# Kernel tuning notes

Hardware: AMD Instinct MI355X
Metric: run time of the kernel (lower is better)

## Reference

```python
import jax, jax.numpy as jnp
import numpy as np

IN_FEATURES = 4096
OUT_FEATURES = 11008
W_BITS = 4
GROUP_SIZE = 128
NUM_CHERRIES = 128                       # ceil(4096*0.03125)//8*8
NUM_NORMAL = IN_FEATURES - NUM_CHERRIES  # 3968
N_GROUPS = NUM_NORMAL // GROUP_SIZE      # 31
QROWS = NUM_NORMAL // 8 * W_BITS         # 1984 packed uint8 rows
QMIN = -(2 ** (W_BITS - 1))              # signed int4 min = -8
BATCH = 64


def setup_inputs() -> dict:
    key = jax.random.key(0)
    k1, k2, k3, k4, k5 = jax.random.split(key, 5)
    x = jax.random.normal(k1, (BATCH, IN_FEATURES), jnp.float32)
    # packed 4-bit weights: two nibbles per uint8, stored as [QROWS, out]
    qweight = jax.random.randint(k2, (QROWS, OUT_FEATURES), 0, 256, jnp.int32).astype(jnp.uint8)
    # per-group scales, stored transposed as [n_groups, out]
    scales = jax.random.uniform(k3, (N_GROUPS, OUT_FEATURES), jnp.float32, 0.005, 0.02)
    # full-precision outlier ('cherry') columns, stored as [num_cherries, out]
    cherry_weight = jax.random.normal(k4, (NUM_CHERRIES, OUT_FEATURES), jnp.float32) * 0.02
    rng = np.random.default_rng(0)
    cherry_indices = jnp.asarray(
        np.sort(rng.choice(IN_FEATURES, NUM_CHERRIES, replace=False)).astype(np.int32))
    bias = jax.random.normal(k5, (OUT_FEATURES,), jnp.float32) * 0.01
    return {"x": x, "qweight": qweight, "cherry_weight": cherry_weight,
            "cherry_indices": cherry_indices, "scales": scales, "bias": bias}


def _normal_indices(cherry_indices):
    # complement of cherry_indices, as in the torch scatter/nonzero construction
    mask = jnp.ones((IN_FEATURES,), dtype=bool).at[cherry_indices].set(False)
    return jnp.nonzero(mask, size=NUM_NORMAL)[0]  # static size -> jit ok


def reference(x, qweight, cherry_weight, cherry_indices, scales, bias):
    # --- unpack 4-bit weights (matches QuantLinear.unpack for w_bits=4) ---
    q = qweight.T                                    # [out, QROWS]
    nib = jnp.stack([q & 0xF, (q >> 4) & 0xF], axis=-1)  # low nibble first
    nib = nib.reshape(OUT_FEATURES, NUM_NORMAL)
    intw = nib.astype(jnp.int32) + QMIN              # signed int4 values
    # --- dequantize: repeat-interleave per-group scales along in dim ---
    s = jnp.repeat(scales.T, GROUP_SIZE, axis=1)     # [out, NUM_NORMAL]
    w_normal = intw.astype(s.dtype) * s              # dequantized normal weight
    # --- merge cherry outlier columns via column-gather on x (same math as
    #     scattering into a full [out, in] weight then x @ W.T) ---
    normal_idx = _normal_indices(cherry_indices)
    out = x[:, normal_idx] @ w_normal.T + x[:, cherry_indices] @ cherry_weight
    return out + bias
```

## Files before the change

### kernel.cpp

```cpp
#include <hip/hip_runtime.h>
#include <hip/hip_bf16.h>
#include <stdint.h>

#define IN_F 4096
#define OUT_F 11008
#define NUM_CH 128
#define NUM_NORM 3968
#define BATCH 64
#define KSPLIT 8
#define KCHUNK (IN_F / KSPLIT)
#define NMEGA (KCHUNK / 128)
#define BS 136

typedef short short8 __attribute__((ext_vector_type(8)));
typedef float float4v __attribute__((ext_vector_type(4)));
typedef int int4v __attribute__((ext_vector_type(4)));

__device__ __forceinline__ unsigned short f2bf(float f) {
    union { float f; unsigned u; } v; v.f = f;
    unsigned u = v.u;
    return (unsigned short)((u + 0x7FFFu + ((u >> 16) & 1u)) >> 16);
}

__device__ __forceinline__ unsigned pk_bf16(float lo, float hi) {
    __hip_bfloat162 h = __float22bfloat162_rn(make_float2(lo, hi));
    union { __hip_bfloat162 h; unsigned u; } c; c.h = h; return c.u;
}

__global__ __launch_bounds__(256) void init_out(
        const float* __restrict__ bias, float* __restrict__ out) {
    const int i = blockIdx.x * 256 + threadIdx.x;
    const int c = i % (OUT_F / 4);
    const float4v b4 = *reinterpret_cast<const float4v*>(bias + c * 4);
    reinterpret_cast<float4v*>(out)[i] = b4;
}

__global__ __launch_bounds__(256) void permute_x(
        const float* __restrict__ x, const int* __restrict__ cidx,
        unsigned short* __restrict__ xp) {
    int i = blockIdx.x * blockDim.x + threadIdx.x;
    int b = blockIdx.y;
    int lo = 0, hi = NUM_CH;
    while (lo < hi) { int mid = (lo + hi) >> 1; if (cidx[mid] < i) lo = mid + 1; else hi = mid; }
    bool isch = (lo < NUM_CH) && (cidx[lo] == i);
    int pos = isch ? (NUM_NORM + lo) : (i - lo);
    xp[b * IN_F + pos] = f2bf(x[b * IN_F + i]);
}

__global__ __launch_bounds__(256, 3) void qgemm(
        const unsigned short* __restrict__ xp, const int* __restrict__ qw,
        const float* __restrict__ cw, const float* __restrict__ scales,
        float* __restrict__ out) {
    __shared__ unsigned short Bt[4][32][BS];

    const int tid  = threadIdx.x;
    const int wave = tid >> 6;
    const int lane = tid & 63;
    const int ln   = lane & 15;
    const int lq   = lane >> 4;
    const int c4   = (lane & 7) * 4;
    const int rg   = lane >> 3;

    const int n0w   = (blockIdx.x * 4 + wave) * 32;
    const int kbase = blockIdx.y * KCHUNK;

    unsigned short (*tile)[BS] = Bt[wave];

    const int*   qcolp = qw + n0w + c4;
    const float* scolp = scales + n0w + c4;
    const float* ccolp = cw + n0w + c4;

    float4v acc[4][2];
    #pragma unroll
    for (int mt = 0; mt < 4; ++mt)
        #pragma unroll
        for (int nf = 0; nf < 2; ++nf) acc[mt][nf] = (float4v){0.f, 0.f, 0.f, 0.f};

    int4v qcur[8]; float4v scur;
    {
        const size_t rb = (size_t)(kbase >> 1) + rg * 8;
        #pragma unroll
        for (int i = 0; i < 8; ++i)
            qcur[i] = *reinterpret_cast<const int4v*>(qcolp + (rb + i) * OUT_F);
        scur = *reinterpret_cast<const float4v*>(scolp + (size_t)(kbase >> 7) * OUT_F);
    }

    for (int s = 0; s < NMEGA; ++s) {
        const int k0 = kbase + s * 128;

        if (k0 < NUM_NORM) {
            int4v q[8]; const float4v sc = scur;
            #pragma unroll
            for (int i = 0; i < 8; ++i) q[i] = qcur[i];
            const int kn = k0 + 128;
            if (s + 1 < NMEGA && kn < NUM_NORM) {
                const size_t rb = (size_t)(kn >> 1) + rg * 8;
                #pragma unroll
                for (int i = 0; i < 8; ++i)
                    qcur[i] = *reinterpret_cast<const int4v*>(qcolp + (rb + i) * OUT_F);
                scur = *reinterpret_cast<const float4v*>(scolp + (size_t)(kn >> 7) * OUT_F);
            }
            #pragma unroll
            for (int j = 0; j < 4; ++j) {
                const float s1 = sc[j];
                #pragma unroll
                for (int p = 0; p < 2; ++p) {
                    union { short8 v; unsigned u[4]; } wv;
                    #pragma unroll
                    for (int m = 0; m < 4; ++m) {
                        const int qq = q[p * 4 + m][j];
                        wv.u[m] = pk_bf16((float)((qq & 0xF) - 8) * s1,
                                          (float)(((qq >> 4) & 0xF) - 8) * s1);
                    }
                    *reinterpret_cast<short8*>(&tile[c4 + j][rg * 16 + p * 8]) = wv.v;
                }
            }
        } else {
            float4v chv[16];
            #pragma unroll
            for (int t = 0; t < 16; ++t)
                chv[t] = *reinterpret_cast<const float4v*>(
                    ccolp + (size_t)(rg * 16 + t) * OUT_F);
            #pragma unroll
            for (int j = 0; j < 4; ++j) {
                #pragma unroll
                for (int p = 0; p < 2; ++p) {
                    union { short8 v; unsigned u[4]; } wv;
                    #pragma unroll
                    for (int m = 0; m < 4; ++m)
                        wv.u[m] = pk_bf16(chv[p * 8 + 2 * m][j], chv[p * 8 + 2 * m + 1][j]);
                    *reinterpret_cast<short8*>(&tile[c4 + j][rg * 16 + p * 8]) = wv.v;
                }
            }
        }

        short8 a_sub[4];
        #pragma unroll
        for (int mt = 0; mt < 4; ++mt)
            a_sub[mt] = *reinterpret_cast<const short8*>(
                xp + (size_t)(mt * 16 + ln) * IN_F + k0 + (lq << 3));

        #pragma unroll
        for (int sub = 0; sub < 4; ++sub) {
            const short8 b0 = *reinterpret_cast<const short8*>(
                &tile[ln][sub * 32 + (lq << 3)]);
            const short8 b1 = *reinterpret_cast<const short8*>(
                &tile[16 + ln][sub * 32 + (lq << 3)]);
            short8 a_nxt[4];
            if (sub < 3) {
                #pragma unroll
                for (int mt = 0; mt < 4; ++mt)
                    a_nxt[mt] = *reinterpret_cast<const short8*>(
                        xp + (size_t)(mt * 16 + ln) * IN_F + k0 + (sub + 1) * 32 + (lq << 3));
            }
            #pragma unroll
            for (int mt = 0; mt < 4; ++mt) {
                acc[mt][0] = __builtin_amdgcn_mfma_f32_16x16x32_bf16(a_sub[mt], b0, acc[mt][0], 0, 0, 0);
                acc[mt][1] = __builtin_amdgcn_mfma_f32_16x16x32_bf16(a_sub[mt], b1, acc[mt][1], 0, 0, 0);
            }
            if (sub < 3) {
                #pragma unroll
                for (int mt = 0; mt < 4; ++mt) a_sub[mt] = a_nxt[mt];
            }
        }
    }

    #pragma unroll
    for (int mt = 0; mt < 4; ++mt) {
        #pragma unroll
        for (int nf = 0; nf < 2; ++nf) {
            const int n = n0w + nf * 16 + ln;
            #pragma unroll
            for (int r = 0; r < 4; ++r) {
                const int m = mt * 16 + (lq << 2) + r;
                atomicAdd(&out[(size_t)m * OUT_F + n], acc[mt][nf][r]);
            }
        }
    }
}

extern "C" void kernel_launch(void* const* d_in, const int* in_sizes, int n_in,
                              void* d_out, int out_size, void* d_ws, size_t ws_size,
                              hipStream_t stream) {
    const float* x      = (const float*)d_in[0];
    const int*   qw     = (const int*)d_in[1];
    const float* cw     = (const float*)d_in[2];
    const int*   cidx   = (const int*)d_in[3];
    const float* scales = (const float*)d_in[4];
    const float* bias   = (const float*)d_in[5];
    float*       out    = (float*)d_out;
    unsigned short* xp  = (unsigned short*)d_ws;

    init_out<<<(BATCH * OUT_F / 4) / 256, 256, 0, stream>>>(bias, out);
    dim3 pgrid(IN_F / 256, BATCH);
    permute_x<<<pgrid, 256, 0, stream>>>(x, cidx, xp);
    qgemm<<<dim3(OUT_F / 128, KSPLIT), 256, 0, stream>>>(xp, qw, cw, scales, out);
}
```

Baseline: 174.8 us.

## Repack weights into MFMA-friendly layout and dequantize directly in registers

Adds two pre-pass kernels that run on every call. One packs the 4-bit weights so that each output column's 16 K-bytes sit contiguously; the other converts the cherry weights to bf16 in a matching per-column layout. The GEMM then loads each lane's B fragment straight from global memory into registers, dequantizes it there and feeds the MFMAs, with no LDS tile and no strided column loads. The cost is an extra full pass over the original weights plus writing and re-reading the packed copy, traded for better-coalesced streaming and a simpler inner loop.

```diff
diff --git a/kernel.cpp b/kernel.cpp
--- a/kernel.cpp
+++ b/kernel.cpp
@@ -7,14 +7,14 @@
 #define NUM_CH 128
 #define NUM_NORM 3968
 #define BATCH 64
+#define KB_N 124
 #define KSPLIT 8
-#define KCHUNK (IN_F / KSPLIT)
-#define NMEGA (KCHUNK / 128)
-#define BS 136
+#define KCHUNK 512
+#define NSUB 16
 
 typedef short short8 __attribute__((ext_vector_type(8)));
 typedef float float4v __attribute__((ext_vector_type(4)));
-typedef int int4v __attribute__((ext_vector_type(4)));
+typedef unsigned uint4v __attribute__((ext_vector_type(4)));
 
 __device__ __forceinline__ unsigned short f2bf(float f) {
     union { float f; unsigned u; } v; v.f = f;
@@ -47,28 +47,84 @@
     xp[b * IN_F + pos] = f2bf(x[b * IN_F + i]);
 }
 
-__global__ __launch_bounds__(256, 3) void qgemm(
-        const unsigned short* __restrict__ xp, const int* __restrict__ qw,
-        const float* __restrict__ cw, const float* __restrict__ scales,
+__global__ __launch_bounds__(256) void repack_n(
+        const int* __restrict__ qw, unsigned char* __restrict__ pk) {
+    const int kb = blockIdx.y;
+    const int n  = blockIdx.x * 256 + threadIdx.x;
+    const int* src = qw + (size_t)kb * 16 * OUT_F + n;
+    unsigned dw[4];
+    #pragma unroll
+    for (int a = 0; a < 4; ++a) {
+        const unsigned b0 = (unsigned)src[(size_t)(4 * a + 0) * OUT_F] & 0xFFu;
+        const unsigned b1 = (unsigned)src[(size_t)(4 * a + 1) * OUT_F] & 0xFFu;
+        const unsigned b2 = (unsigned)src[(size_t)(4 * a + 2) * OUT_F] & 0xFFu;
+        const unsigned b3 = (unsigned)src[(size_t)(4 * a + 3) * OUT_F] & 0xFFu;
+        dw[a] = b0 | (b1 << 8) | (b2 << 16) | (b3 << 24);
+    }
+    *reinterpret_cast<uint4v*>(pk + ((size_t)kb * OUT_F + n) * 16) =
+        (uint4v){dw[0], dw[1], dw[2], dw[3]};
+}
+
+__global__ __launch_bounds__(256) void repack_ch(
+        const float* __restrict__ cw, unsigned short* __restrict__ pkc) {
+    const int kbc = blockIdx.y;
+    const int n   = blockIdx.x * 256 + threadIdx.x;
+    const float* src = cw + (size_t)kbc * 32 * OUT_F + n;
+    unsigned u[16];
+    #pragma unroll
+    for (int j = 0; j < 16; ++j)
+        u[j] = pk_bf16(src[(size_t)(2 * j) * OUT_F], src[(size_t)(2 * j + 1) * OUT_F]);
+    uint4v* dst = reinterpret_cast<uint4v*>(pkc + ((size_t)kbc * OUT_F + n) * 32);
+    #pragma unroll
+    for (int q = 0; q < 4; ++q)
+        dst[q] = (uint4v){u[4 * q], u[4 * q + 1], u[4 * q + 2], u[4 * q + 3]};
+}
+
+__global__ __launch_bounds__(256) void qgemm(
+        const unsigned short* __restrict__ xp, const unsigned* __restrict__ pk,
+        const unsigned short* __restrict__ pkc, const float* __restrict__ scales,
         float* __restrict__ out) {
-    __shared__ unsigned short Bt[4][32][BS];
-
     const int tid  = threadIdx.x;
     const int wave = tid >> 6;
     const int lane = tid & 63;
     const int ln   = lane & 15;
     const int lq   = lane >> 4;
-    const int c4   = (lane & 7) * 4;
-    const int rg   = lane >> 3;
-
-    const int n0w   = (blockIdx.x * 4 + wave) * 32;
-    const int kbase = blockIdx.y * KCHUNK;
-
-    unsigned short (*tile)[BS] = Bt[wave];
-
-    const int*   qcolp = qw + n0w + c4;
-    const float* scolp = scales + n0w + c4;
-    const float* ccolp = cw + n0w + c4;
+    const int n0w  = (blockIdx.x * 4 + wave) * 32;
+    const int ky   = blockIdx.y;
+    const int kbase = ky * KCHUNK;
+    const int kb0   = ky * 16;
+    const bool chblk = (ky == KSPLIT - 1);
+    const int nsubn  = chblk ? 12 : 16;
+
+    const int nc0 = n0w + ln;
+    const int nc1 = n0w + 16 + ln;
+
+    unsigned bq[16][2];
+    #pragma unroll
+    for (int sub = 0; sub < 16; ++sub) {
+        if (sub < nsubn) {
+            bq[sub][0] = pk[((size_t)(kb0 + sub) * OUT_F + nc0) * 4 + lq];
+            bq[sub][1] = pk[((size_t)(kb0 + sub) * OUT_F + nc1) * 4 + lq];
+        }
+    }
+    short8 cb[4][2];
+    if (chblk) {
+        #pragma unroll
+        for (int s4 = 0; s4 < 4; ++s4) {
+            cb[s4][0] = *reinterpret_cast<const short8*>(
+                pkc + ((size_t)s4 * OUT_F + nc0) * 32 + lq * 8);
+            cb[s4][1] = *reinterpret_cast<const short8*>(
+                pkc + ((size_t)s4 * OUT_F + nc1) * 32 + lq * 8);
+        }
+    }
+    float sc[4][2];
+    #pragma unroll
+    for (int gi = 0; gi < 4; ++gi) {
+        if (gi * 4 < nsubn) {
+            sc[gi][0] = scales[(size_t)(ky * 4 + gi) * OUT_F + nc0];
+            sc[gi][1] = scales[(size_t)(ky * 4 + gi) * OUT_F + nc1];
+        }
+    }
 
     float4v acc[4][2];
     #pragma unroll
@@ -76,92 +132,45 @@
         #pragma unroll
         for (int nf = 0; nf < 2; ++nf) acc[mt][nf] = (float4v){0.f, 0.f, 0.f, 0.f};
 
-    int4v qcur[8]; float4v scur;
-    {
-        const size_t rb = (size_t)(kbase >> 1) + rg * 8;
-        #pragma unroll
-        for (int i = 0; i < 8; ++i)
-            qcur[i] = *reinterpret_cast<const int4v*>(qcolp + (rb + i) * OUT_F);
-        scur = *reinterpret_cast<const float4v*>(scolp + (size_t)(kbase >> 7) * OUT_F);
-    }
-
-    for (int s = 0; s < NMEGA; ++s) {
-        const int k0 = kbase + s * 128;
-
-        if (k0 < NUM_NORM) {
-            int4v q[8]; const float4v sc = scur;
-            #pragma unroll
-            for (int i = 0; i < 8; ++i) q[i] = qcur[i];
-            const int kn = k0 + 128;
-            if (s + 1 < NMEGA && kn < NUM_NORM) {
-                const size_t rb = (size_t)(kn >> 1) + rg * 8;
-                #pragma unroll
-                for (int i = 0; i < 8; ++i)
-                    qcur[i] = *reinterpret_cast<const int4v*>(qcolp + (rb + i) * OUT_F);
-                scur = *reinterpret_cast<const float4v*>(scolp + (size_t)(kn >> 7) * OUT_F);
+    const unsigned short* xpb = xp + kbase + lq * 8;
+    short8 a_cur[4], a_nxt[4];
+    #pragma unroll
+    for (int mt = 0; mt < 4; ++mt)
+        a_cur[mt] = *reinterpret_cast<const short8*>(xpb + (size_t)(mt * 16 + ln) * IN_F);
+
+    #pragma unroll
+    for (int sub = 0; sub < 16; ++sub) {
+        short8 bf0, bf1;
+        if (!chblk || sub < 12) {
+            const float s0 = sc[sub >> 2][0], s1 = sc[sub >> 2][1];
+            union { short8 v; unsigned u[4]; } w0, w1;
+            #pragma unroll
+            for (int i = 0; i < 4; ++i) {
+                const unsigned y0 = (bq[sub][0] >> (8 * i)) & 0xFFu;
+                const unsigned y1 = (bq[sub][1] >> (8 * i)) & 0xFFu;
+                w0.u[i] = pk_bf16((float)((int)(y0 & 0xFu) - 8) * s0,
+                                  (float)((int)(y0 >> 4) - 8) * s0);
+                w1.u[i] = pk_bf16((float)((int)(y1 & 0xFu) - 8) * s1,
+                                  (float)((int)(y1 >> 4) - 8) * s1);
             }
-            #pragma unroll
-            for (int j = 0; j < 4; ++j) {
-                const float s1 = sc[j];
-                #pragma unroll
-                for (int p = 0; p < 2; ++p) {
-                    union { short8 v; unsigned u[4]; } wv;
-                    #pragma unroll
-                    for (int m = 0; m < 4; ++m) {
-                        const int qq = q[p * 4 + m][j];
-                        wv.u[m] = pk_bf16((float)((qq & 0xF) - 8) * s1,
-                                          (float)(((qq >> 4) & 0xF) - 8) * s1);
-                    }
-                    *reinterpret_cast<short8*>(&tile[c4 + j][rg * 16 + p * 8]) = wv.v;
-                }
-            }
+            bf0 = w0.v; bf1 = w1.v;
         } else {
-            float4v chv[16];
-            #pragma unroll
-            for (int t = 0; t < 16; ++t)
-                chv[t] = *reinterpret_cast<const float4v*>(
-                    ccolp + (size_t)(rg * 16 + t) * OUT_F);
-            #pragma unroll
-            for (int j = 0; j < 4; ++j) {
-                #pragma unroll
-                for (int p = 0; p < 2; ++p) {
-                    union { short8 v; unsigned u[4]; } wv;
-                    #pragma unroll
-                    for (int m = 0; m < 4; ++m)
-                        wv.u[m] = pk_bf16(chv[p * 8 + 2 * m][j], chv[p * 8 + 2 * m + 1][j]);
-                    *reinterpret_cast<short8*>(&tile[c4 + j][rg * 16 + p * 8]) = wv.v;
-                }
-            }
-        }
-
-        short8 a_sub[4];
-        #pragma unroll
-        for (int mt = 0; mt < 4; ++mt)
-            a_sub[mt] = *reinterpret_cast<const short8*>(
-                xp + (size_t)(mt * 16 + ln) * IN_F + k0 + (lq << 3));
-
-        #pragma unroll
-        for (int sub = 0; sub < 4; ++sub) {
-            const short8 b0 = *reinterpret_cast<const short8*>(
-                &tile[ln][sub * 32 + (lq << 3)]);
-            const short8 b1 = *reinterpret_cast<const short8*>(
-                &tile[16 + ln][sub * 32 + (lq << 3)]);
-            short8 a_nxt[4];
-            if (sub < 3) {
-                #pragma unroll
-                for (int mt = 0; mt < 4; ++mt)
-                    a_nxt[mt] = *reinterpret_cast<const short8*>(
-                        xp + (size_t)(mt * 16 + ln) * IN_F + k0 + (sub + 1) * 32 + (lq << 3));
-            }
-            #pragma unroll
-            for (int mt = 0; mt < 4; ++mt) {
-                acc[mt][0] = __builtin_amdgcn_mfma_f32_16x16x32_bf16(a_sub[mt], b0, acc[mt][0], 0, 0, 0);
-                acc[mt][1] = __builtin_amdgcn_mfma_f32_16x16x32_bf16(a_sub[mt], b1, acc[mt][1], 0, 0, 0);
-            }
-            if (sub < 3) {
-                #pragma unroll
-                for (int mt = 0; mt < 4; ++mt) a_sub[mt] = a_nxt[mt];
-            }
+            bf0 = cb[sub - 12][0]; bf1 = cb[sub - 12][1];
+        }
+        if (sub < 15) {
+            #pragma unroll
+            for (int mt = 0; mt < 4; ++mt)
+                a_nxt[mt] = *reinterpret_cast<const short8*>(
+                    xpb + (size_t)(mt * 16 + ln) * IN_F + (sub + 1) * 32);
+        }
+        #pragma unroll
+        for (int mt = 0; mt < 4; ++mt) {
+            acc[mt][0] = __builtin_amdgcn_mfma_f32_16x16x32_bf16(a_cur[mt], bf0, acc[mt][0], 0, 0, 0);
+            acc[mt][1] = __builtin_amdgcn_mfma_f32_16x16x32_bf16(a_cur[mt], bf1, acc[mt][1], 0, 0, 0);
+        }
+        if (sub < 15) {
+            #pragma unroll
+            for (int mt = 0; mt < 4; ++mt) a_cur[mt] = a_nxt[mt];
         }
     }
 
@@ -189,10 +198,17 @@
     const float* scales = (const float*)d_in[4];
     const float* bias   = (const float*)d_in[5];
     float*       out    = (float*)d_out;
+
     unsigned short* xp  = (unsigned short*)d_ws;
+    unsigned char*  pkn = (unsigned char*)d_ws + (512 << 10);
+    unsigned short* pkc = (unsigned short*)((char*)d_ws + (512 << 10)
+                              + (size_t)KB_N * OUT_F * 16);
 
     init_out<<<(BATCH * OUT_F / 4) / 256, 256, 0, stream>>>(bias, out);
     dim3 pgrid(IN_F / 256, BATCH);
     permute_x<<<pgrid, 256, 0, stream>>>(x, cidx, xp);
-    qgemm<<<dim3(OUT_F / 128, KSPLIT), 256, 0, stream>>>(xp, qw, cw, scales, out);
-}
+    repack_n<<<dim3(OUT_F / 256, KB_N), 256, 0, stream>>>(qw, pkn);
+    repack_ch<<<dim3(OUT_F / 256, 4), 256, 0, stream>>>(cw, pkc);
+    qgemm<<<dim3(OUT_F / 128, KSPLIT), 256, 0, stream>>>(
+        xp, (const unsigned*)pkn, pkc, scales, out);
+}
```

After: 196.3 us. 1.12x slower.
